# Optimization experiments

Measured on AMD Instinct MI355X. Metric: run time of the kernel, lower is better.

The kernel has to match this reference:

```python
import jax, jax.numpy as jnp
import numpy as np

B, S, H, KVH, D = 1, 2048, 32, 8, 128
HID = 4096
THETA = 10000.0
LCK = 2  # number of cached draft steps before this call
SCALE = D ** -0.5
NEG = -1e9


def _rope_tables(pos):
    # pos: [B,S] int -> cos,sin [B,S,D]
    inv_freq = 1.0 / (THETA ** (jnp.arange(0, D, 2, dtype=jnp.float32) / D))
    ang = pos.astype(jnp.float32)[..., None] * inv_freq  # [B,S,D/2]
    emb = jnp.concatenate([ang, ang], axis=-1)
    return jnp.cos(emb), jnp.sin(emb)


def _rotate_half(x):
    x1, x2 = jnp.split(x, 2, axis=-1)
    return jnp.concatenate([-x2, x1], axis=-1)


def setup_inputs() -> dict:
    key = jax.random.key(0)
    ks = jax.random.split(key, 10)
    causal = jnp.where(jnp.tril(jnp.ones((S, S), dtype=bool)), 0.0, NEG).astype(jnp.float32)
    return {
        "combined_states": jax.random.normal(ks[0], (B, S, 2 * HID), dtype=jnp.float32),
        "attention_mask": jnp.broadcast_to(causal, (B, 1, S, S)),
        "position_ids": jnp.broadcast_to(jnp.arange(S, dtype=jnp.int32), (B, S)),
        "cache_k0": jax.random.normal(ks[1], (B, H, S, D), dtype=jnp.float32),
        "cache_k1": jax.random.normal(ks[2], (B, H, S, D), dtype=jnp.float32),
        "cache_v0": jax.random.normal(ks[3], (B, H, S, D), dtype=jnp.float32),
        "cache_v1": jax.random.normal(ks[4], (B, H, S, D), dtype=jnp.float32),
        "Wq": jax.random.normal(ks[5], (2 * HID, H * D), dtype=jnp.float32) * 0.02,
        "Wk": jax.random.normal(ks[6], (2 * HID, KVH * D), dtype=jnp.float32) * 0.02,
        "Wv": jax.random.normal(ks[7], (2 * HID, KVH * D), dtype=jnp.float32) * 0.02,
        "Wo": jax.random.normal(ks[8], (H * D, HID), dtype=jnp.float32) * 0.02,
    }


def reference(combined_states, attention_mask, position_ids,
              cache_k0, cache_k1, cache_v0, cache_v1, Wq, Wk, Wv, Wo):
    # projections (weights stored [in, out])
    q = (combined_states @ Wq).reshape(B, S, H, D).transpose(0, 2, 1, 3)   # [B,H,S,D]
    k = (combined_states @ Wk).reshape(B, S, KVH, D).transpose(0, 2, 1, 3)  # [B,KVH,S,D]
    v = (combined_states @ Wv).reshape(B, S, KVH, D).transpose(0, 2, 1, 3)

    # RoPE shifted by lck tokens into the future
    cos, sin = _rope_tables(position_ids + LCK)
    cos = cos[:, None]  # [B,1,S,D]
    sin = sin[:, None]
    q = q * cos + _rotate_half(q) * sin
    k = k * cos + _rotate_half(k) * sin

    # GQA expand (repeat_interleave on head dim)
    groups = H // KVH
    k = jnp.repeat(k, groups, axis=1)  # [B,H,S,D]
    v = jnp.repeat(v, groups, axis=1)

    # cache_hidden after append: K = [cache_k0, cache_k1, k], V likewise (new_lck = 3)
    # full causal attention against step-0 keys
    aw0 = jnp.einsum("bhqd,bhkd->bhqk", q, cache_k0) * SCALE + attention_mask  # [B,H,S,S]
    # diagonal per-step contributions for i >= 1
    d1 = jnp.einsum("bhsd,bhsd->bhs", q, cache_k1) * SCALE
    d2 = jnp.einsum("bhsd,bhsd->bhs", q, k) * SCALE
    attn_weights = jnp.concatenate([aw0, d1[..., None], d2[..., None]], axis=-1)  # [B,H,S,S+2]

    probs = jax.nn.softmax(attn_weights.astype(jnp.float32), axis=-1).astype(q.dtype)

    attn_out = jnp.einsum("bhqk,bhkd->bhqd", probs[..., :S], cache_v0)
    attn_out = attn_out + probs[..., S, None] * cache_v1
    attn_out = attn_out + probs[..., S + 1, None] * v

    attn_out = attn_out.transpose(0, 2, 1, 3).reshape(B, S, H * D)
    return attn_out @ Wo
```

## Files before the change

kernel.cpp:

```cpp
#include <hip/hip_runtime.h>

#define S_LEN 2048
#define NH    32
#define NKV   8
#define DH    128
#define QDIM  4096
#define KVDIM 1024
#define K2H   8192
#define SCALE_F 0.08838834764831845f

typedef __attribute__((ext_vector_type(8))) short short8;
typedef __attribute__((ext_vector_type(4))) float f32x4;

__device__ __forceinline__ ushort f2bf(float f){
  union { float f; unsigned u; } x; x.f = f;
  unsigned r = (x.u + 0x7FFFu + ((x.u>>16)&1u)) >> 16;
  return (ushort)r;
}
__device__ __forceinline__ float bf2f(ushort h){
  union { unsigned u; float f; } x; x.u = ((unsigned)h)<<16; return x.f;
}

__global__ void cast_f32_bf16(const float* __restrict__ in, ushort* __restrict__ out, int n4){
  int i = blockIdx.x*256 + threadIdx.x;
  if (i >= n4) return;
  float4 v = ((const float4*)in)[i];
  ushort4 o; o.x=f2bf(v.x); o.y=f2bf(v.y); o.z=f2bf(v.z); o.w=f2bf(v.w);
  ((ushort4*)out)[i] = o;
}

__global__ void transpose_cast(const float* __restrict__ in, ushort* __restrict__ out, int K, int N){
  __shared__ float tile[32][33];
  int n0 = blockIdx.x<<5, k0 = blockIdx.y<<5;
  int tx = threadIdx.x, ty = threadIdx.y;
  #pragma unroll
  for (int j=0;j<4;++j)
    tile[ty+8*j][tx] = in[(size_t)(k0+ty+8*j)*N + n0 + tx];
  __syncthreads();
  #pragma unroll
  for (int j=0;j<4;++j)
    out[(size_t)(n0+ty+8*j)*K + k0 + tx] = f2bf(tile[tx][ty+8*j]);
}

__global__ void transpose_v0(const float* __restrict__ v0, ushort* __restrict__ v0t){
  __shared__ float tile[32][33];
  int s0 = blockIdx.x<<5, d0 = blockIdx.y<<5, h = blockIdx.z;
  int tx = threadIdx.x, ty = threadIdx.y;
  #pragma unroll
  for (int j=0;j<4;++j)
    tile[ty+8*j][tx] = v0[((size_t)h*S_LEN + s0+ty+8*j)*DH + d0 + tx];
  __syncthreads();
  #pragma unroll
  for (int j=0;j<4;++j)
    v0t[((size_t)h*DH + d0+ty+8*j)*S_LEN + s0 + tx] = f2bf(tile[tx][ty+8*j]);
}

__global__ void rope_cast(const float* __restrict__ pre, const int* __restrict__ pids,
                          ushort* __restrict__ outb, int nheads, int total){
  int idx = blockIdx.x*256 + threadIdx.x;
  if (idx >= total) return;
  int d = idx & 63; int r = idx >> 6;
  int h = r % nheads; int s = r / nheads;
  size_t base = ((size_t)s*nheads + h)*DH;
  float a = pre[base + d], b = pre[base + d + 64];
  float pos = (float)(pids[s] + 2);
  float ang = pos * exp2f(-(float)d * 0.20762050593046014f);
  float sn, cs; sincosf(ang, &sn, &cs);
  outb[base + d]      = f2bf(a*cs - b*sn);
  outb[base + d + 64] = f2bf(b*cs + a*sn);
}

__global__ __launch_bounds__(256) void gemm_bf16(
    const ushort* __restrict__ A, const ushort* __restrict__ Bt,
    float* __restrict__ C, int M, int N, int K)
{
  __shared__ __align__(16) ushort As[128*64];
  __shared__ __align__(16) ushort Bs[128*64];
  const int tid = threadIdx.x;
  const int w = tid>>6, lane = tid&63;
  const int wm = w>>1, wn = w&1;
  const int lg = lane>>4, lr = lane&15;
  const int m0 = blockIdx.y<<7, n0 = blockIdx.x<<7;
  f32x4 acc[4][4];
  #pragma unroll
  for (int mt=0;mt<4;++mt)
    #pragma unroll
    for (int nt=0;nt<4;++nt) acc[mt][nt] = (f32x4){0.f,0.f,0.f,0.f};

  for (int k0=0;k0<K;k0+=64){
    __syncthreads();
    #pragma unroll
    for (int i=0;i<4;++i){
      int c = i*256+tid; int row = c>>3, ch = c&7;
      short8 av = *(const short8*)(A + (size_t)(m0+row)*K + k0 + ch*8);
      *(short8*)((char*)As + row*128 + ((ch<<4) ^ ((row&7)<<4))) = av;
      short8 bv = *(const short8*)(Bt + (size_t)(n0+row)*K + k0 + ch*8);
      *(short8*)((char*)Bs + row*128 + ((ch<<4) ^ ((row&7)<<4))) = bv;
    }
    __syncthreads();
    #pragma unroll
    for (int ks=0;ks<2;++ks){
      short8 af[4], bfr[4];
      #pragma unroll
      for (int mt=0;mt<4;++mt){
        int row = (wm<<6)+(mt<<4)+lr;
        af[mt] = *(const short8*)((char*)As + row*128 + (((ks<<6)+(lg<<4)) ^ ((row&7)<<4)));
      }
      #pragma unroll
      for (int nt=0;nt<4;++nt){
        int row = (wn<<6)+(nt<<4)+lr;
        bfr[nt] = *(const short8*)((char*)Bs + row*128 + (((ks<<6)+(lg<<4)) ^ ((row&7)<<4)));
      }
      #pragma unroll
      for (int mt=0;mt<4;++mt)
        #pragma unroll
        for (int nt=0;nt<4;++nt)
          acc[mt][nt] = __builtin_amdgcn_mfma_f32_16x16x32_bf16(af[mt], bfr[nt], acc[mt][nt], 0,0,0);
    }
  }
  #pragma unroll
  for (int mt=0;mt<4;++mt)
    #pragma unroll
    for (int nt=0;nt<4;++nt)
      #pragma unroll
      for (int r=0;r<4;++r){
        int row = m0 + (wm<<6) + (mt<<4) + (lg<<2) + r;
        int col = n0 + (wn<<6) + (nt<<4) + lr;
        C[(size_t)row*N + col] = acc[mt][nt][r];
      }
}

__global__ __launch_bounds__(256) void attn_kernel(
    const ushort* __restrict__ qb,
    const ushort* __restrict__ kb,
    const float* __restrict__ k1c,
    const float* __restrict__ v1c,
    const float* __restrict__ k0c,
    const ushort* __restrict__ v0t,
    const float* __restrict__ vpre,
    ushort* __restrict__ outb)
{
  __shared__ __align__(16) ushort Ks[64*128];
  __shared__ __align__(16) ushort Vs[128*64];
  __shared__ __align__(16) ushort Ps[4][16*64];
  const int tid = threadIdx.x;
  const int w = tid>>6, lane = tid&63;
  const int lg = lane>>4, lr = lane&15;
  const int h = blockIdx.y, kvh = h>>2;
  const int q0 = blockIdx.x<<6, qbase = q0 + (w<<4);

  short8 qf[4];
  {
    int row = qbase + lr;
    const ushort* qr = qb + ((size_t)row*NH + h)*DH;
    #pragma unroll
    for (int ks=0;ks<4;++ks) qf[ks] = *(const short8*)(qr + ks*32 + lg*8);
  }

  float d1v[4], d2v[4];
  #pragma unroll
  for (int r=0;r<4;++r){
    int row = qbase + (lg<<2) + r;
    const ushort* qr  = qb  + ((size_t)row*NH  + h  )*DH + lr*8;
    const float*  kr1 = k1c + ((size_t)h*S_LEN + row)*DH + lr*8;
    const ushort* kr2 = kb  + ((size_t)row*NKV + kvh)*DH + lr*8;
    float s1=0.f, s2=0.f;
    #pragma unroll
    for (int j=0;j<8;++j){
      float qv = bf2f(qr[j]);
      s1 = fmaf(qv, kr1[j], s1);
      s2 = fmaf(qv, bf2f(kr2[j]), s2);
    }
    #pragma unroll
    for (int mm=1;mm<16;mm<<=1){ s1 += __shfl_xor(s1,mm,64); s2 += __shfl_xor(s2,mm,64); }
    d1v[r] = s1*SCALE_F; d2v[r] = s2*SCALE_F;
  }

  f32x4 o[8];
  #pragma unroll
  for (int dt=0;dt<8;++dt) o[dt] = (f32x4){0.f,0.f,0.f,0.f};
  float mrow[4], lrow[4];
  #pragma unroll
  for (int r=0;r<4;++r){ mrow[r] = -1e30f; lrow[r] = 0.f; }

  const int ntiles = blockIdx.x + 1;
  for (int kt=0; kt<ntiles; ++kt){
    const int key0 = kt<<6;
    __syncthreads();
    #pragma unroll
    for (int i=0;i<4;++i){
      int c = i*256 + tid;
      int krow = c>>4, ch = c&15;
      const float* src = k0c + ((size_t)h*S_LEN + key0 + krow)*DH + ch*8;
      float4 fa = *(const float4*)src;
      float4 fb = *(const float4*)(src+4);
      short8 pk;
      pk[0]=(short)f2bf(fa.x); pk[1]=(short)f2bf(fa.y);
      pk[2]=(short)f2bf(fa.z); pk[3]=(short)f2bf(fa.w);
      pk[4]=(short)f2bf(fb.x); pk[5]=(short)f2bf(fb.y);
      pk[6]=(short)f2bf(fb.z); pk[7]=(short)f2bf(fb.w);
      *(short8*)((char*)Ks + krow*256 + ((ch<<4) ^ ((krow&7)<<4))) = pk;
    }
    #pragma unroll
    for (int i=0;i<4;++i){
      int c = i*256 + tid;
      int drow = c>>3, ch = c&7;
      short8 vv = *(const short8*)(v0t + ((size_t)h*DH + drow)*S_LEN + key0 + ch*8);
      *(short8*)((char*)Vs + drow*128 + ((ch<<4) ^ ((drow&7)<<4))) = vv;
    }
    __syncthreads();

    f32x4 sc[4];
    #pragma unroll
    for (int nt=0;nt<4;++nt) sc[nt] = (f32x4){0.f,0.f,0.f,0.f};
    #pragma unroll
    for (int ks=0;ks<4;++ks){
      #pragma unroll
      for (int nt=0;nt<4;++nt){
        int krow = (nt<<4) + lr;
        short8 kf = *(const short8*)((char*)Ks + krow*256 + (((ks<<6)+(lg<<4)) ^ ((krow&7)<<4)));
        sc[nt] = __builtin_amdgcn_mfma_f32_16x16x32_bf16(qf[ks], kf, sc[nt], 0,0,0);
      }
    }

    #pragma unroll
    for (int r=0;r<4;++r){
      int qrow = qbase + (lg<<2) + r;
      float vals[4]; float mx = -1e30f;
      #pragma unroll
      for (int nt=0;nt<4;++nt){
        int key = key0 + (nt<<4) + lr;
        float v = sc[nt][r]*SCALE_F;
        if (key > qrow) v = -1e30f;
        vals[nt] = v; mx = fmaxf(mx, v);
      }
      #pragma unroll
      for (int mm=1;mm<16;mm<<=1) mx = fmaxf(mx, __shfl_xor(mx,mm,64));
      float mn = fmaxf(mrow[r], mx);
      float alpha = __expf(mrow[r]-mn);
      float ls = 0.f;
      int qr = (lg<<2)+r;
      #pragma unroll
      for (int nt=0;nt<4;++nt){
        float p = __expf(vals[nt]-mn);
        ls += p;
        *(ushort*)((char*)&Ps[w][0] + ((qr<<7) + (((((nt<<4)+lr))<<1) ^ ((qr&7)<<4)))) = f2bf(p);
      }
      #pragma unroll
      for (int mm=1;mm<16;mm<<=1) ls += __shfl_xor(ls,mm,64);
      lrow[r] = lrow[r]*alpha + ls;
      mrow[r] = mn;
      #pragma unroll
      for (int dt=0;dt<8;++dt) o[dt][r] *= alpha;
    }

    #pragma unroll
    for (int ks=0;ks<2;++ks){
      short8 pa = *(const short8*)((char*)&Ps[w][0] + ((lr<<7) + (((ks<<6)+(lg<<4)) ^ ((lr&7)<<4))));
      #pragma unroll
      for (int dt=0;dt<8;++dt){
        int drow = (dt<<4) + lr;
        short8 vb = *(const short8*)((char*)Vs + drow*128 + (((ks<<6)+(lg<<4)) ^ ((drow&7)<<4)));
        o[dt] = __builtin_amdgcn_mfma_f32_16x16x32_bf16(pa, vb, o[dt], 0,0,0);
      }
    }
  }

  #pragma unroll
  for (int r=0;r<4;++r){
    int qrow = qbase + (lg<<2) + r;
    float mfin = fmaxf(mrow[r], fmaxf(d1v[r], d2v[r]));
    float alpha = __expf(mrow[r]-mfin);
    float p1 = __expf(d1v[r]-mfin);
    float p2 = __expf(d2v[r]-mfin);
    float linv = 1.0f / (lrow[r]*alpha + p1 + p2);
    const float* v1r = v1c + ((size_t)h*S_LEN + qrow)*DH;
    const float* vpr = vpre + (size_t)qrow*KVDIM + kvh*DH;
    ushort* outr = outb + (size_t)qrow*QDIM + h*DH;
    #pragma unroll
    for (int dt=0;dt<8;++dt){
      int d = (dt<<4) + lr;
      float val = (o[dt][r]*alpha + p1*v1r[d] + p2*vpr[d]) * linv;
      outr[d] = f2bf(val);
    }
  }
}

extern "C" void kernel_launch(void* const* d_in, const int* in_sizes, int n_in,
                              void* d_out, int out_size, void* d_ws, size_t ws_size,
                              hipStream_t stream) {
  const float* X    = (const float*)d_in[0];
  const int*   pids = (const int*)  d_in[2];
  const float* k0   = (const float*)d_in[3];
  const float* k1   = (const float*)d_in[4];
  const float* v0   = (const float*)d_in[5];
  const float* v1   = (const float*)d_in[6];
  const float* Wq   = (const float*)d_in[7];
  const float* Wk   = (const float*)d_in[8];
  const float* Wv   = (const float*)d_in[9];
  const float* Wo   = (const float*)d_in[10];
  float* out = (float*)d_out;

  char* ws = (char*)d_ws;
  ushort* Xb   = (ushort*)(ws);
  ushort* WT   = (ushort*)(ws + 33554432);
  float*  qpre = (float*) (ws + 100663296);
  float*  kpre = (float*) (ws + 134217728);
  float*  vpre = (float*) (ws + 142606336);
  ushort* qbv  = (ushort*)(ws + 150994944);
  ushort* kbv  = (ushort*)(ws + 167772160);
  ushort* v0t  = (ushort*)(ws + 171966464);
  ushort* attnb = (ushort*)qpre;

  dim3 b256(256), b328(32,8);

  cast_f32_bf16<<<16384, b256, 0, stream>>>(X, Xb, (S_LEN*K2H)/4);

  transpose_cast<<<dim3(QDIM/32, K2H/32), b328, 0, stream>>>(Wq, WT, K2H, QDIM);
  gemm_bf16<<<dim3(QDIM/128, S_LEN/128), b256, 0, stream>>>(Xb, WT, qpre, S_LEN, QDIM, K2H);
  transpose_cast<<<dim3(KVDIM/32, K2H/32), b328, 0, stream>>>(Wk, WT, K2H, KVDIM);
  gemm_bf16<<<dim3(KVDIM/128, S_LEN/128), b256, 0, stream>>>(Xb, WT, kpre, S_LEN, KVDIM, K2H);
  transpose_cast<<<dim3(KVDIM/32, K2H/32), b328, 0, stream>>>(Wv, WT, K2H, KVDIM);
  gemm_bf16<<<dim3(KVDIM/128, S_LEN/128), b256, 0, stream>>>(Xb, WT, vpre, S_LEN, KVDIM, K2H);

  rope_cast<<<16384, b256, 0, stream>>>(qpre, pids, qbv, NH,  S_LEN*NH*64);
  rope_cast<<<4096,  b256, 0, stream>>>(kpre, pids, kbv, NKV, S_LEN*NKV*64);

  transpose_v0<<<dim3(S_LEN/32, DH/32, NH), b328, 0, stream>>>(v0, v0t);

  attn_kernel<<<dim3(S_LEN/64, NH), b256, 0, stream>>>(qbv, kbv, k1, v1, k0, v0t, vpre, attnb);

  transpose_cast<<<dim3(QDIM/32, QDIM/32), b328, 0, stream>>>(Wo, WT, QDIM, QDIM);
  gemm_bf16<<<dim3(QDIM/128, S_LEN/128), b256, 0, stream>>>(attnb, WT, out, S_LEN, QDIM, QDIM);
}
```

Baseline: 1.186 ms.

## Use direct global-to-LDS loads, fuse K/V GEMMs, balance causal attention tiles

The GEMM and attention tile loads now go through global_load_lds (direct global-to-LDS copies) with a pre-swizzled source column, replacing register-staged stores. The K and V projections are merged into one GEMM over a concatenated transposed weight, and cache_k0 is cast to bf16 once up front rather than converted on every attention tile load. Each attention block now handles a mirrored pair of query tiles to balance the causal workload, and transpose_cast processes 64-row tiles with packed stores. The aim is fewer launches, less conversion work and less register traffic, at the cost of an extra cast pass and more complex addressing.

Measured after the change: 970.7 us. 18.1% less time.

```diff
diff --git a/kernel.cpp b/kernel.cpp
--- a/kernel.cpp
+++ b/kernel.cpp
@@ -6,7 +6,9 @@
 #define DH    128
 #define QDIM  4096
 #define KVDIM 1024
+#define KV2   2048
 #define K2H   8192
+#define NT    32
 #define SCALE_F 0.08838834764831845f
 
 typedef __attribute__((ext_vector_type(8))) short short8;
@@ -19,6 +21,12 @@
 }
 __device__ __forceinline__ float bf2f(ushort h){
   union { unsigned u; float f; } x; x.u = ((unsigned)h)<<16; return x.f;
+}
+
+__device__ __forceinline__ void gload16(const void* g, void* l){
+  __builtin_amdgcn_global_load_lds(
+      (const __attribute__((address_space(1))) unsigned*)g,
+      (__attribute__((address_space(3))) unsigned*)l, 16, 0, 0);
 }
 
 __global__ void cast_f32_bf16(const float* __restrict__ in, ushort* __restrict__ out, int n4){
@@ -30,16 +38,19 @@
 }
 
 __global__ void transpose_cast(const float* __restrict__ in, ushort* __restrict__ out, int K, int N){
-  __shared__ float tile[32][33];
-  int n0 = blockIdx.x<<5, k0 = blockIdx.y<<5;
+  __shared__ float tile[64][33];
+  int n0 = blockIdx.x<<5, k0 = blockIdx.y<<6;
   int tx = threadIdx.x, ty = threadIdx.y;
   #pragma unroll
-  for (int j=0;j<4;++j)
+  for (int j=0;j<8;++j)
     tile[ty+8*j][tx] = in[(size_t)(k0+ty+8*j)*N + n0 + tx];
   __syncthreads();
   #pragma unroll
-  for (int j=0;j<4;++j)
-    out[(size_t)(n0+ty+8*j)*K + k0 + tx] = f2bf(tile[tx][ty+8*j]);
+  for (int j=0;j<4;++j){
+    int c = ty+8*j;
+    ushort2 o; o.x = f2bf(tile[2*tx][c]); o.y = f2bf(tile[2*tx+1][c]);
+    *(ushort2*)(out + (size_t)(n0+c)*K + k0 + 2*tx) = o;
+  }
 }
 
 __global__ void transpose_v0(const float* __restrict__ v0, ushort* __restrict__ v0t){
@@ -56,18 +67,19 @@
 }
 
 __global__ void rope_cast(const float* __restrict__ pre, const int* __restrict__ pids,
-                          ushort* __restrict__ outb, int nheads, int total){
+                          ushort* __restrict__ outb, int nheads, int istride, int total){
   int idx = blockIdx.x*256 + threadIdx.x;
   if (idx >= total) return;
   int d = idx & 63; int r = idx >> 6;
   int h = r % nheads; int s = r / nheads;
-  size_t base = ((size_t)s*nheads + h)*DH;
-  float a = pre[base + d], b = pre[base + d + 64];
+  const float* src = pre + (size_t)s*istride + h*DH;
+  float a = src[d], b = src[d+64];
   float pos = (float)(pids[s] + 2);
   float ang = pos * exp2f(-(float)d * 0.20762050593046014f);
   float sn, cs; sincosf(ang, &sn, &cs);
-  outb[base + d]      = f2bf(a*cs - b*sn);
-  outb[base + d + 64] = f2bf(b*cs + a*sn);
+  ushort* dst = outb + ((size_t)s*nheads + h)*DH;
+  dst[d]      = f2bf(a*cs - b*sn);
+  dst[d+64]   = f2bf(b*cs + a*sn);
 }
 
 __global__ __launch_bounds__(256) void gemm_bf16(
@@ -81,6 +93,11 @@
   const int wm = w>>1, wn = w&1;
   const int lg = lane>>4, lr = lane&15;
   const int m0 = blockIdx.y<<7, n0 = blockIdx.x<<7;
+  const int g = lane>>3, cc = lane&7;
+  const int sc = (cc ^ g) << 3;
+  const ushort* Abase = A + (size_t)(m0 + w*32 + g)*K + sc;
+  const ushort* Bbase = Bt + (size_t)(n0 + w*32 + g)*K + sc;
+
   f32x4 acc[4][4];
   #pragma unroll
   for (int mt=0;mt<4;++mt)
@@ -91,11 +108,8 @@
     __syncthreads();
     #pragma unroll
     for (int i=0;i<4;++i){
-      int c = i*256+tid; int row = c>>3, ch = c&7;
-      short8 av = *(const short8*)(A + (size_t)(m0+row)*K + k0 + ch*8);
-      *(short8*)((char*)As + row*128 + ((ch<<4) ^ ((row&7)<<4))) = av;
-      short8 bv = *(const short8*)(Bt + (size_t)(n0+row)*K + k0 + ch*8);
-      *(short8*)((char*)Bs + row*128 + ((ch<<4) ^ ((row&7)<<4))) = bv;
+      gload16(Abase + k0 + (size_t)(i*8)*K, As + (w*32 + i*8)*64);
+      gload16(Bbase + k0 + (size_t)(i*8)*K, Bs + (w*32 + i*8)*64);
     }
     __syncthreads();
     #pragma unroll
@@ -104,12 +118,12 @@
       #pragma unroll
       for (int mt=0;mt<4;++mt){
         int row = (wm<<6)+(mt<<4)+lr;
-        af[mt] = *(const short8*)((char*)As + row*128 + (((ks<<6)+(lg<<4)) ^ ((row&7)<<4)));
+        af[mt] = *(const short8*)((char*)As + row*128 + (((ks<<6)+(lg<<4)) ^ ((lr&7)<<4)));
       }
       #pragma unroll
       for (int nt=0;nt<4;++nt){
         int row = (wn<<6)+(nt<<4)+lr;
-        bfr[nt] = *(const short8*)((char*)Bs + row*128 + (((ks<<6)+(lg<<4)) ^ ((row&7)<<4)));
+        bfr[nt] = *(const short8*)((char*)Bs + row*128 + (((ks<<6)+(lg<<4)) ^ ((lr&7)<<4)));
       }
       #pragma unroll
       for (int mt=0;mt<4;++mt)
@@ -135,7 +149,7 @@
     const ushort* __restrict__ kb,
     const float* __restrict__ k1c,
     const float* __restrict__ v1c,
-    const float* __restrict__ k0c,
+    const ushort* __restrict__ k0b,
     const ushort* __restrict__ v0t,
     const float* __restrict__ vpre,
     ushort* __restrict__ outb)
@@ -147,141 +161,140 @@
   const int w = tid>>6, lane = tid&63;
   const int lg = lane>>4, lr = lane&15;
   const int h = blockIdx.y, kvh = h>>2;
-  const int q0 = blockIdx.x<<6, qbase = q0 + (w<<4);
-
-  short8 qf[4];
-  {
-    int row = qbase + lr;
-    const ushort* qr = qb + ((size_t)row*NH + h)*DH;
-    #pragma unroll
-    for (int ks=0;ks<4;++ks) qf[ks] = *(const short8*)(qr + ks*32 + lg*8);
-  }
-
-  float d1v[4], d2v[4];
-  #pragma unroll
-  for (int r=0;r<4;++r){
-    int row = qbase + (lg<<2) + r;
-    const ushort* qr  = qb  + ((size_t)row*NH  + h  )*DH + lr*8;
-    const float*  kr1 = k1c + ((size_t)h*S_LEN + row)*DH + lr*8;
-    const ushort* kr2 = kb  + ((size_t)row*NKV + kvh)*DH + lr*8;
-    float s1=0.f, s2=0.f;
-    #pragma unroll
-    for (int j=0;j<8;++j){
-      float qv = bf2f(qr[j]);
-      s1 = fmaf(qv, kr1[j], s1);
-      s2 = fmaf(qv, bf2f(kr2[j]), s2);
-    }
-    #pragma unroll
-    for (int mm=1;mm<16;mm<<=1){ s1 += __shfl_xor(s1,mm,64); s2 += __shfl_xor(s2,mm,64); }
-    d1v[r] = s1*SCALE_F; d2v[r] = s2*SCALE_F;
-  }
-
-  f32x4 o[8];
-  #pragma unroll
-  for (int dt=0;dt<8;++dt) o[dt] = (f32x4){0.f,0.f,0.f,0.f};
-  float mrow[4], lrow[4];
-  #pragma unroll
-  for (int r=0;r<4;++r){ mrow[r] = -1e30f; lrow[r] = 0.f; }
-
-  const int ntiles = blockIdx.x + 1;
-  for (int kt=0; kt<ntiles; ++kt){
-    const int key0 = kt<<6;
-    __syncthreads();
-    #pragma unroll
-    for (int i=0;i<4;++i){
-      int c = i*256 + tid;
-      int krow = c>>4, ch = c&15;
-      const float* src = k0c + ((size_t)h*S_LEN + key0 + krow)*DH + ch*8;
-      float4 fa = *(const float4*)src;
-      float4 fb = *(const float4*)(src+4);
-      short8 pk;
-      pk[0]=(short)f2bf(fa.x); pk[1]=(short)f2bf(fa.y);
-      pk[2]=(short)f2bf(fa.z); pk[3]=(short)f2bf(fa.w);
-      pk[4]=(short)f2bf(fb.x); pk[5]=(short)f2bf(fb.y);
-      pk[6]=(short)f2bf(fb.z); pk[7]=(short)f2bf(fb.w);
-      *(short8*)((char*)Ks + krow*256 + ((ch<<4) ^ ((krow&7)<<4))) = pk;
-    }
-    #pragma unroll
-    for (int i=0;i<4;++i){
-      int c = i*256 + tid;
-      int drow = c>>3, ch = c&7;
-      short8 vv = *(const short8*)(v0t + ((size_t)h*DH + drow)*S_LEN + key0 + ch*8);
-      *(short8*)((char*)Vs + drow*128 + ((ch<<4) ^ ((drow&7)<<4))) = vv;
-    }
-    __syncthreads();
-
-    f32x4 sc[4];
-    #pragma unroll
-    for (int nt=0;nt<4;++nt) sc[nt] = (f32x4){0.f,0.f,0.f,0.f};
-    #pragma unroll
-    for (int ks=0;ks<4;++ks){
-      #pragma unroll
-      for (int nt=0;nt<4;++nt){
-        int krow = (nt<<4) + lr;
-        short8 kf = *(const short8*)((char*)Ks + krow*256 + (((ks<<6)+(lg<<4)) ^ ((krow&7)<<4)));
-        sc[nt] = __builtin_amdgcn_mfma_f32_16x16x32_bf16(qf[ks], kf, sc[nt], 0,0,0);
+  const int g4 = lane>>4, c16 = lane&15;
+  const int g8 = lane>>3, c8 = lane&7;
+
+  for (int rep=0; rep<2; ++rep){
+    const int qt = rep ? (NT-1-(int)blockIdx.x) : (int)blockIdx.x;
+    const int q0 = qt<<6, qbase = q0 + (w<<4);
+
+    short8 qf[4];
+    {
+      int row = qbase + lr;
+      const ushort* qr = qb + ((size_t)row*NH + h)*DH;
+      #pragma unroll
+      for (int ks=0;ks<4;++ks) qf[ks] = *(const short8*)(qr + ks*32 + lg*8);
+    }
+
+    float d1v[4], d2v[4];
+    #pragma unroll
+    for (int r=0;r<4;++r){
+      int row = qbase + (lg<<2) + r;
+      const ushort* qr  = qb  + ((size_t)row*NH  + h  )*DH + lr*8;
+      const float*  kr1 = k1c + ((size_t)h*S_LEN + row)*DH + lr*8;
+      const ushort* kr2 = kb  + ((size_t)row*NKV + kvh)*DH + lr*8;
+      float s1=0.f, s2=0.f;
+      #pragma unroll
+      for (int j=0;j<8;++j){
+        float qv = bf2f(qr[j]);
+        s1 = fmaf(qv, kr1[j], s1);
+        s2 = fmaf(qv, bf2f(kr2[j]), s2);
+      }
+      #pragma unroll
+      for (int mm=1;mm<16;mm<<=1){ s1 += __shfl_xor(s1,mm,64); s2 += __shfl_xor(s2,mm,64); }
+      d1v[r] = s1*SCALE_F; d2v[r] = s2*SCALE_F;
+    }
+
+    f32x4 o[8];
+    #pragma unroll
+    for (int dt=0;dt<8;++dt) o[dt] = (f32x4){0.f,0.f,0.f,0.f};
+    float mrow[4], lrow[4];
+    #pragma unroll
+    for (int r=0;r<4;++r){ mrow[r] = -1e30f; lrow[r] = 0.f; }
+
+    const int ntiles = qt + 1;
+    for (int kt=0; kt<ntiles; ++kt){
+      const int key0 = kt<<6;
+      __syncthreads();
+      #pragma unroll
+      for (int i=0;i<4;++i){
+        int row = (w<<4) + (i<<2) + g4;
+        int scol = (c16 ^ (((i<<2)+g4)&7)) << 3;
+        gload16(k0b + ((size_t)h*S_LEN + key0 + row)*DH + scol,
+                Ks + ((w<<4)+(i<<2))*128);
+      }
+      #pragma unroll
+      for (int i=0;i<4;++i){
+        int row = (w<<5) + (i<<3) + g8;
+        int scol = (c8 ^ g8) << 3;
+        gload16(v0t + ((size_t)h*DH + row)*S_LEN + key0 + scol,
+                Vs + ((w<<5)+(i<<3))*64);
+      }
+      __syncthreads();
+
+      f32x4 sc[4];
+      #pragma unroll
+      for (int nt=0;nt<4;++nt) sc[nt] = (f32x4){0.f,0.f,0.f,0.f};
+      #pragma unroll
+      for (int ks=0;ks<4;++ks){
+        #pragma unroll
+        for (int nt=0;nt<4;++nt){
+          int krow = (nt<<4) + lr;
+          short8 kf = *(const short8*)((char*)Ks + krow*256 + (((ks<<6)+(lg<<4)) ^ ((krow&7)<<4)));
+          sc[nt] = __builtin_amdgcn_mfma_f32_16x16x32_bf16(qf[ks], kf, sc[nt], 0,0,0);
+        }
+      }
+
+      #pragma unroll
+      for (int r=0;r<4;++r){
+        int qrow = qbase + (lg<<2) + r;
+        float vals[4]; float mx = -1e30f;
+        #pragma unroll
+        for (int nt=0;nt<4;++nt){
+          int key = key0 + (nt<<4) + lr;
+          float v = sc[nt][r]*SCALE_F;
+          if (key > qrow) v = -1e30f;
+          vals[nt] = v; mx = fmaxf(mx, v);
+        }
+        #pragma unroll
+        for (int mm=1;mm<16;mm<<=1) mx = fmaxf(mx, __shfl_xor(mx,mm,64));
+        float mn = fmaxf(mrow[r], mx);
+        float alpha = __expf(mrow[r]-mn);
+        float ls = 0.f;
+        int qr = (lg<<2)+r;
+        #pragma unroll
+        for (int nt=0;nt<4;++nt){
+          float p = __expf(vals[nt]-mn);
+          ls += p;
+          *(ushort*)((char*)&Ps[w][0] + ((qr<<7) + ((((nt<<4)+lr)<<1) ^ ((qr&7)<<4)))) = f2bf(p);
+        }
+        #pragma unroll
+        for (int mm=1;mm<16;mm<<=1) ls += __shfl_xor(ls,mm,64);
+        lrow[r] = lrow[r]*alpha + ls;
+        mrow[r] = mn;
+        #pragma unroll
+        for (int dt=0;dt<8;++dt) o[dt][r] *= alpha;
+      }
+
+      #pragma unroll
+      for (int ks=0;ks<2;++ks){
+        short8 pa = *(const short8*)((char*)&Ps[w][0] + ((lr<<7) + (((ks<<6)+(lg<<4)) ^ ((lr&7)<<4))));
+        #pragma unroll
+        for (int dt=0;dt<8;++dt){
+          int drow = (dt<<4) + lr;
+          short8 vb = *(const short8*)((char*)Vs + drow*128 + (((ks<<6)+(lg<<4)) ^ ((drow&7)<<4)));
+          o[dt] = __builtin_amdgcn_mfma_f32_16x16x32_bf16(pa, vb, o[dt], 0,0,0);
+        }
       }
     }
 
     #pragma unroll
     for (int r=0;r<4;++r){
       int qrow = qbase + (lg<<2) + r;
-      float vals[4]; float mx = -1e30f;
-      #pragma unroll
-      for (int nt=0;nt<4;++nt){
-        int key = key0 + (nt<<4) + lr;
-        float v = sc[nt][r]*SCALE_F;
-        if (key > qrow) v = -1e30f;
-        vals[nt] = v; mx = fmaxf(mx, v);
-      }
-      #pragma unroll
-      for (int mm=1;mm<16;mm<<=1) mx = fmaxf(mx, __shfl_xor(mx,mm,64));
-      float mn = fmaxf(mrow[r], mx);
-      float alpha = __expf(mrow[r]-mn);
-      float ls = 0.f;
-      int qr = (lg<<2)+r;
-      #pragma unroll
-      for (int nt=0;nt<4;++nt){
-        float p = __expf(vals[nt]-mn);
-        ls += p;
-        *(ushort*)((char*)&Ps[w][0] + ((qr<<7) + (((((nt<<4)+lr))<<1) ^ ((qr&7)<<4)))) = f2bf(p);
-      }
-      #pragma unroll
-      for (int mm=1;mm<16;mm<<=1) ls += __shfl_xor(ls,mm,64);
-      lrow[r] = lrow[r]*alpha + ls;
-      mrow[r] = mn;
-      #pragma unroll
-      for (int dt=0;dt<8;++dt) o[dt][r] *= alpha;
-    }
-
-    #pragma unroll
-    for (int ks=0;ks<2;++ks){
-      short8 pa = *(const short8*)((char*)&Ps[w][0] + ((lr<<7) + (((ks<<6)+(lg<<4)) ^ ((lr&7)<<4))));
+      float mfin = fmaxf(mrow[r], fmaxf(d1v[r], d2v[r]));
+      float alpha = __expf(mrow[r]-mfin);
+      float p1 = __expf(d1v[r]-mfin);
+      float p2 = __expf(d2v[r]-mfin);
+      float linv = 1.0f / (lrow[r]*alpha + p1 + p2);
+      const float* v1r = v1c + ((size_t)h*S_LEN + qrow)*DH;
+      const float* vpr = vpre + (size_t)qrow*KV2 + kvh*DH;
+      ushort* outr = outb + (size_t)qrow*QDIM + h*DH;
       #pragma unroll
       for (int dt=0;dt<8;++dt){
-        int drow = (dt<<4) + lr;
-        short8 vb = *(const short8*)((char*)Vs + drow*128 + (((ks<<6)+(lg<<4)) ^ ((drow&7)<<4)));
-        o[dt] = __builtin_amdgcn_mfma_f32_16x16x32_bf16(pa, vb, o[dt], 0,0,0);
-      }
-    }
-  }
-
-  #pragma unroll
-  for (int r=0;r<4;++r){
-    int qrow = qbase + (lg<<2) + r;
-    float mfin = fmaxf(mrow[r], fmaxf(d1v[r], d2v[r]));
-    float alpha = __expf(mrow[r]-mfin);
-    float p1 = __expf(d1v[r]-mfin);
-    float p2 = __expf(d2v[r]-mfin);
-    float linv = 1.0f / (lrow[r]*alpha + p1 + p2);
-    const float* v1r = v1c + ((size_t)h*S_LEN + qrow)*DH;
-    const float* vpr = vpre + (size_t)qrow*KVDIM + kvh*DH;
-    ushort* outr = outb + (size_t)qrow*QDIM + h*DH;
-    #pragma unroll
-    for (int dt=0;dt<8;++dt){
-      int d = (dt<<4) + lr;
-      float val = (o[dt][r]*alpha + p1*v1r[d] + p2*vpr[d]) * linv;
-      outr[d] = f2bf(val);
+        int d = (dt<<4) + lr;
+        float val = (o[dt][r]*alpha + p1*v1r[d] + p2*vpr[d]) * linv;
+        outr[d] = f2bf(val);
+      }
     }
   }
 }
@@ -302,34 +315,39 @@
   float* out = (float*)d_out;
 
   char* ws = (char*)d_ws;
-  ushort* Xb   = (ushort*)(ws);
-  ushort* WT   = (ushort*)(ws + 33554432);
-  float*  qpre = (float*) (ws + 100663296);
-  float*  kpre = (float*) (ws + 134217728);
-  float*  vpre = (float*) (ws + 142606336);
-  ushort* qbv  = (ushort*)(ws + 150994944);
-  ushort* kbv  = (ushort*)(ws + 167772160);
-  ushort* v0t  = (ushort*)(ws + 171966464);
+  ushort* Xb    = (ushort*)(ws);
+  ushort* WT0   = (ushort*)(ws + 33554432);
+  ushort* k0b   = WT0;
+  ushort* WoT   = (ushort*)(ws + 67108864);
+  float*  qpre  = (float*) (ws + 100663296);
+  float*  kvpre = (float*) (ws + 134217728);
+  ushort* qbv   = (ushort*)(ws + 150994944);
+  ushort* kbv   = (ushort*)(ws + 167772160);
+  ushort* v0t   = (ushort*)(ws + 171966464);
   ushort* attnb = (ushort*)qpre;
 
   dim3 b256(256), b328(32,8);
 
   cast_f32_bf16<<<16384, b256, 0, stream>>>(X, Xb, (S_LEN*K2H)/4);
 
-  transpose_cast<<<dim3(QDIM/32, K2H/32), b328, 0, stream>>>(Wq, WT, K2H, QDIM);
-  gemm_bf16<<<dim3(QDIM/128, S_LEN/128), b256, 0, stream>>>(Xb, WT, qpre, S_LEN, QDIM, K2H);
-  transpose_cast<<<dim3(KVDIM/32, K2H/32), b328, 0, stream>>>(Wk, WT, K2H, KVDIM);
-  gemm_bf16<<<dim3(KVDIM/128, S_LEN/128), b256, 0, stream>>>(Xb, WT, kpre, S_LEN, KVDIM, K2H);
-  transpose_cast<<<dim3(KVDIM/32, K2H/32), b328, 0, stream>>>(Wv, WT, K2H, KVDIM);
-  gemm_bf16<<<dim3(KVDIM/128, S_LEN/128), b256, 0, stream>>>(Xb, WT, vpre, S_LEN, KVDIM, K2H);
-
-  rope_cast<<<16384, b256, 0, stream>>>(qpre, pids, qbv, NH,  S_LEN*NH*64);
-  rope_cast<<<4096,  b256, 0, stream>>>(kpre, pids, kbv, NKV, S_LEN*NKV*64);
+  transpose_cast<<<dim3(QDIM/32, K2H/64), b328, 0, stream>>>(Wq, WT0, K2H, QDIM);
+  gemm_bf16<<<dim3(QDIM/128, S_LEN/128), b256, 0, stream>>>(Xb, WT0, qpre, S_LEN, QDIM, K2H);
+
+  transpose_cast<<<dim3(KVDIM/32, K2H/64), b328, 0, stream>>>(Wk, WT0, K2H, KVDIM);
+  transpose_cast<<<dim3(KVDIM/32, K2H/64), b328, 0, stream>>>(Wv, WT0 + (size_t)KVDIM*K2H, K2H, KVDIM);
+  gemm_bf16<<<dim3(KV2/128, S_LEN/128), b256, 0, stream>>>(Xb, WT0, kvpre, S_LEN, KV2, K2H);
+
+  cast_f32_bf16<<<8192, b256, 0, stream>>>(k0, k0b, (NH*S_LEN*DH)/4);
+
+  transpose_cast<<<dim3(QDIM/32, QDIM/64), b328, 0, stream>>>(Wo, WoT, QDIM, QDIM);
+
+  rope_cast<<<16384, b256, 0, stream>>>(qpre,  pids, qbv, NH,  QDIM, S_LEN*NH*64);
+  rope_cast<<<4096,  b256, 0, stream>>>(kvpre, pids, kbv, NKV, KV2,  S_LEN*NKV*64);
 
   transpose_v0<<<dim3(S_LEN/32, DH/32, NH), b328, 0, stream>>>(v0, v0t);
 
-  attn_kernel<<<dim3(S_LEN/64, NH), b256, 0, stream>>>(qbv, kbv, k1, v1, k0, v0t, vpre, attnb);
-
-  transpose_cast<<<dim3(QDIM/32, QDIM/32), b328, 0, stream>>>(Wo, WT, QDIM, QDIM);
-  gemm_bf16<<<dim3(QDIM/128, S_LEN/128), b256, 0, stream>>>(attnb, WT, out, S_LEN, QDIM, QDIM);
-}
+  attn_kernel<<<dim3(NT/2, NH), b256, 0, stream>>>(qbv, kbv, k1, v1, k0b, v0t,
+                                                   kvpre + KVDIM, attnb);
+
+  gemm_bf16<<<dim3(QDIM/128, S_LEN/128), b256, 0, stream>>>(attnb, WoT, out, S_LEN, QDIM, QDIM);
+}
```
